# Kernel optimization log

Hardware: AMD Instinct MI355X
Metric: run time of the kernel (lower is better)

The kernel has to match this reference:

```python
import jax, jax.numpy as jnp
import numpy as np

B, T, F, H = 8192, 96, 64, 256


def setup_inputs() -> dict:
    key = jax.random.key(0)
    ks = jax.random.split(key, 8)
    s = 0.05
    return {
        "decoder_feature": jax.random.normal(ks[0], (B, T, F), jnp.float32),
        "init_state": jax.random.normal(ks[1], (B, H), jnp.float32),
        "decoder_init_input": jax.random.normal(ks[2], (B, 1), jnp.float32),
        "kernel": jax.random.normal(ks[3], (1 + F, 3 * H), jnp.float32) * s,
        "recurrent_kernel": jax.random.normal(ks[4], (H, 3 * H), jnp.float32) * s,
        "input_bias": jnp.zeros((3 * H,), jnp.float32),
        "recurrent_bias": jnp.zeros((3 * H,), jnp.float32),
        "dense_w": jax.random.normal(ks[5], (H, 1), jnp.float32) * s,
        "dense_b": jnp.zeros((1,), jnp.float32),
        "predict_seq_length": T,
    }


def reference(decoder_feature, init_state, decoder_init_input, kernel,
              recurrent_kernel, input_bias, recurrent_bias, dense_w, dense_b,
              predict_seq_length):
    # teacher=None, use_attention=False path of Decoder2.forward.
    # Keras GRUCell (reset_after=True) recurrence, scanned over time.
    feats = jnp.swapaxes(decoder_feature[:, :predict_seq_length, :], 0, 1)  # [T,B,F]

    def step(carry, feat_t):
        prev_out, h = carry                                   # [B,1], [B,H]
        x = jnp.concatenate([prev_out, feat_t], axis=-1)      # [B,1+F]
        mx = x @ kernel + input_bias                          # [B,3H]
        mh = h @ recurrent_kernel + recurrent_bias            # [B,3H]
        xz, xr, xh = jnp.split(mx, 3, axis=-1)
        hz, hr, hh = jnp.split(mh, 3, axis=-1)
        z = jax.nn.sigmoid(xz + hz)
        r = jax.nn.sigmoid(xr + hr)
        cand = jnp.tanh(xh + r * hh)
        h_new = z * h + (1.0 - z) * cand
        out = h_new @ dense_w + dense_b                       # [B,1]
        return (out, h_new), out

    _, outs = jax.lax.scan(step, (decoder_init_input, init_state), feats)
    return jnp.swapaxes(outs, 0, 1)                           # [B,T,1]
```

## Files before the change

### kernel.cpp

```cpp
#include <hip/hip_runtime.h>


#define Bdim 8192
#define Tdim 96
#define Fdim 64
#define Hdim 256
#define BM   32
#define XS   72
#define HS   264
#define OS   97

typedef __attribute__((ext_vector_type(8))) short s16x8;
typedef __attribute__((ext_vector_type(4))) float f32x4;

#define MFMA __builtin_amdgcn_mfma_f32_16x16x32_bf16

__device__ __forceinline__ unsigned short f2bf(float f) {
    union { float f; unsigned u; } v; v.f = f;
    unsigned r = v.u + 0x7FFFu + ((v.u >> 16) & 1u);
    return (unsigned short)(r >> 16);
}

__global__ void prep_swz(const float* __restrict__ Wk, const float* __restrict__ Wr,
                         unsigned short* __restrict__ sW) {
    int idx = blockIdx.x * blockDim.x + threadIdx.x;
    if (idx >= 480 * 64) return;
    int lane = idx & 63, f = idx >> 6;
    int n2 = f & 1;
    int g  = (f >> 1) % 3;
    int kt = (f / 6) % 10;
    int w  = f / 60;
    int q = lane >> 4, cc = lane & 15;
    int n = g * 256 + w * 32 + n2 * 16 + cc;
    unsigned short* d = sW + (size_t)idx * 8;
#pragma unroll
    for (int j = 0; j < 8; ++j) {
        float v;
        if (kt < 8) v = Wr[(size_t)(kt * 32 + q * 8 + j) * 768 + n];
        else        v = Wk[(size_t)(1 + (kt - 8) * 32 + q * 8 + j) * 768 + n];
        d[j] = f2bf(v);
    }
}

__launch_bounds__(512, 2)
__global__ void gru_mfma5(
    const float* __restrict__ feat,
    const float* __restrict__ init_state,
    const float* __restrict__ init_inp,
    const unsigned short* __restrict__ sW,
    const float* __restrict__ Wk,
    const float* __restrict__ ib, const float* __restrict__ rb,
    const float* __restrict__ dw, const float* __restrict__ db,
    float* __restrict__ out)
{
    __shared__ __align__(16) unsigned short xs[BM * XS];
    __shared__ __align__(16) unsigned short hs[BM * HS];
    __shared__ float wpart[2][8][BM];
    __shared__ float outbuf[BM * OS];

    const int tid  = threadIdx.x;
    const int lane = tid & 63;
    const int w    = tid >> 6;
    const int q    = lane >> 4;
    const int c    = lane & 15;
    const int b0   = blockIdx.x * BM;

    float bz[2], brr[2], bxh[2], bhh[2], wk0z[2], wk0r[2], wk0h[2], dwv[2];
#pragma unroll
    for (int n2 = 0; n2 < 2; ++n2) {
        int col = w * 32 + n2 * 16 + c;
        bz[n2]   = ib[col]       + rb[col];
        brr[n2]  = ib[256 + col] + rb[256 + col];
        bxh[n2]  = ib[512 + col];
        bhh[n2]  = rb[512 + col];
        wk0z[n2] = Wk[col];
        wk0r[n2] = Wk[256 + col];
        wk0h[n2] = Wk[512 + col];
        dwv[n2]  = dw[col];
    }
    const float dbv = db[0];

    float hreg[2][2][4];
    float prevreg[2][4];
#pragma unroll
    for (int mt = 0; mt < 2; ++mt)
#pragma unroll
        for (int i = 0; i < 4; ++i) {
            int row = mt * 16 + q * 4 + i;
            prevreg[mt][i] = init_inp[b0 + row];
#pragma unroll
            for (int n2 = 0; n2 < 2; ++n2) {
                int col = w * 32 + n2 * 16 + c;
                float v = init_state[(size_t)(b0 + row) * Hdim + col];
                hreg[mt][n2][i] = v;
                hs[row * HS + col] = f2bf(v);
            }
        }

    {
        int r = tid >> 4, fi = tid & 15;
        float4 f = *(const float4*)&feat[((size_t)(b0 + r) * Tdim + 0) * Fdim + fi * 4];
        ushort4 p; p.x = f2bf(f.x); p.y = f2bf(f.y); p.z = f2bf(f.z); p.w = f2bf(f.w);
        *(ushort4*)&xs[r * XS + fi * 4] = p;
    }

    const unsigned short* wp0 = sW + (size_t)(w * 60) * 512 + lane * 8;

    __syncthreads();

    for (int t = 0; t < Tdim; ++t) {
        f32x4 az[2][2], arr[2][2], axh[2][2], ahh[2][2];
#pragma unroll
        for (int mt = 0; mt < 2; ++mt)
#pragma unroll
            for (int n2 = 0; n2 < 2; ++n2) {
                az[mt][n2] = (f32x4)0.0f; arr[mt][n2] = (f32x4)0.0f;
                axh[mt][n2] = (f32x4)0.0f; ahh[mt][n2] = (f32x4)0.0f;
            }

#pragma unroll
        for (int kt = 0; kt < 10; ++kt) {
            const unsigned short* fp = wp0 + (size_t)(kt * 6) * 512;
            s16x8 b00 = *(const s16x8*)(fp + 0 * 512);
            s16x8 b01 = *(const s16x8*)(fp + 1 * 512);
            s16x8 b10 = *(const s16x8*)(fp + 2 * 512);
            s16x8 b11 = *(const s16x8*)(fp + 3 * 512);
            s16x8 b20 = *(const s16x8*)(fp + 4 * 512);
            s16x8 b21 = *(const s16x8*)(fp + 5 * 512);
            s16x8 a0, a1;
            if (kt < 8) {
                a0 = *(const s16x8*)&hs[c * HS + kt * 32 + q * 8];
                a1 = *(const s16x8*)&hs[(16 + c) * HS + kt * 32 + q * 8];
            } else {
                a0 = *(const s16x8*)&xs[c * XS + (kt - 8) * 32 + q * 8];
                a1 = *(const s16x8*)&xs[(16 + c) * XS + (kt - 8) * 32 + q * 8];
            }
            az[0][0]  = MFMA(a0, b00, az[0][0], 0, 0, 0);
            az[1][0]  = MFMA(a1, b00, az[1][0], 0, 0, 0);
            az[0][1]  = MFMA(a0, b01, az[0][1], 0, 0, 0);
            az[1][1]  = MFMA(a1, b01, az[1][1], 0, 0, 0);
            arr[0][0] = MFMA(a0, b10, arr[0][0], 0, 0, 0);
            arr[1][0] = MFMA(a1, b10, arr[1][0], 0, 0, 0);
            arr[0][1] = MFMA(a0, b11, arr[0][1], 0, 0, 0);
            arr[1][1] = MFMA(a1, b11, arr[1][1], 0, 0, 0);
            if (kt < 8) {
                ahh[0][0] = MFMA(a0, b20, ahh[0][0], 0, 0, 0);
                ahh[1][0] = MFMA(a1, b20, ahh[1][0], 0, 0, 0);
                ahh[0][1] = MFMA(a0, b21, ahh[0][1], 0, 0, 0);
                ahh[1][1] = MFMA(a1, b21, ahh[1][1], 0, 0, 0);
            } else {
                axh[0][0] = MFMA(a0, b20, axh[0][0], 0, 0, 0);
                axh[1][0] = MFMA(a1, b20, axh[1][0], 0, 0, 0);
                axh[0][1] = MFMA(a0, b21, axh[0][1], 0, 0, 0);
                axh[1][1] = MFMA(a1, b21, axh[1][1], 0, 0, 0);
            }
        }
        __syncthreads();

        if (t > 0) {
            int r = lane & 31;
            float s = dbv;
            const float (*wp)[BM] = wpart[(t - 1) & 1];
#pragma unroll
            for (int ww = 0; ww < 8; ++ww) s += wp[ww][r];
            if (w == 0 && lane < 32) outbuf[r * OS + (t - 1)] = s;
#pragma unroll
            for (int mt = 0; mt < 2; ++mt)
#pragma unroll
                for (int i = 0; i < 4; ++i)
                    prevreg[mt][i] = __shfl(s, mt * 16 + q * 4 + i, 64);
        }

        float sd[2][4];
#pragma unroll
        for (int mt = 0; mt < 2; ++mt)
#pragma unroll
            for (int i = 0; i < 4; ++i) sd[mt][i] = 0.0f;

#pragma unroll
        for (int mt = 0; mt < 2; ++mt)
#pragma unroll
            for (int n2 = 0; n2 < 2; ++n2)
#pragma unroll
                for (int i = 0; i < 4; ++i) {
                    float pv = prevreg[mt][i];
                    float zz = 1.0f / (1.0f + __expf(-(az[mt][n2][i] + bz[n2] + pv * wk0z[n2])));
                    float rr = 1.0f / (1.0f + __expf(-(arr[mt][n2][i] + brr[n2] + pv * wk0r[n2])));
                    float cd = tanhf(axh[mt][n2][i] + bxh[n2] + pv * wk0h[n2] +
                                     rr * (ahh[mt][n2][i] + bhh[n2]));
                    float hn = zz * hreg[mt][n2][i] + (1.0f - zz) * cd;
                    hreg[mt][n2][i] = hn;
                    hs[(mt * 16 + q * 4 + i) * HS + w * 32 + n2 * 16 + c] = f2bf(hn);
                    sd[mt][i] += hn * dwv[n2];
                }

#pragma unroll
        for (int mt = 0; mt < 2; ++mt)
#pragma unroll
            for (int i = 0; i < 4; ++i) {
                float s = sd[mt][i];
                s += __shfl_xor(s, 1, 64);
                s += __shfl_xor(s, 2, 64);
                s += __shfl_xor(s, 4, 64);
                s += __shfl_xor(s, 8, 64);
                if (c == 0) wpart[t & 1][w][mt * 16 + q * 4 + i] = s;
            }

        if (t + 1 < Tdim) {
            int r = tid >> 4, fi = tid & 15;
            float4 f = *(const float4*)&feat[((size_t)(b0 + r) * Tdim + (t + 1)) * Fdim + fi * 4];
            ushort4 p; p.x = f2bf(f.x); p.y = f2bf(f.y); p.z = f2bf(f.z); p.w = f2bf(f.w);
            *(ushort4*)&xs[r * XS + fi * 4] = p;
        }
        __syncthreads();
    }

    {
        int r = lane & 31;
        float s = dbv;
        const float (*wp)[BM] = wpart[(Tdim - 1) & 1];
#pragma unroll
        for (int ww = 0; ww < 8; ++ww) s += wp[ww][r];
        if (w == 0 && lane < 32) outbuf[r * OS + (Tdim - 1)] = s;
    }
    __syncthreads();

    for (int i = tid; i < BM * Tdim; i += 512) {
        int r = i / Tdim, tt = i - r * Tdim;
        out[(size_t)b0 * Tdim + i] = outbuf[r * OS + tt];
    }
}

extern "C" void kernel_launch(void* const* d_in, const int* in_sizes, int n_in,
                              void* d_out, int out_size, void* d_ws, size_t ws_size,
                              hipStream_t stream) {
    const float* feat       = (const float*)d_in[0];
    const float* init_state = (const float*)d_in[1];
    const float* init_inp   = (const float*)d_in[2];
    const float* Wk         = (const float*)d_in[3];
    const float* Wr         = (const float*)d_in[4];
    const float* ib         = (const float*)d_in[5];
    const float* rb         = (const float*)d_in[6];
    const float* dw         = (const float*)d_in[7];
    const float* db         = (const float*)d_in[8];
    float* out              = (float*)d_out;

    unsigned short* sW = (unsigned short*)d_ws;

    prep_swz<<<120, 256, 0, stream>>>(Wk, Wr, sW);
    gru_mfma5<<<Bdim / BM, 512, 0, stream>>>(
        feat, init_state, init_inp, sW, Wk, ib, rb, dw, db, out);
}
```

Before: 1.727 ms.

## Halve batch tile to 16 rows with 4 waves each owning 64 hidden columns

Changes the GRU block from 32 batch rows and 8 waves to 16 rows and 4 waves, each wave now computing 64 hidden columns across all three gates. The weight swizzle is re-laid out to match, so each wave issues more MFMAs per A-fragment and the grid doubles to 512 blocks. Biases and the previous-output term are now folded into the accumulator initialisation, and the previous-output reduction moves to the start of the step. The cost is that every block re-streams the full weight matrix from global/L2 for half as many rows, doubling weight traffic per batch element, while register pressure rises from 12 B-fragments held per k-step.

```diff
diff --git a/kernel.cpp b/kernel.cpp
--- a/kernel.cpp
+++ b/kernel.cpp
@@ -5,7 +5,7 @@
 #define Tdim 96
 #define Fdim 64
 #define Hdim 256
-#define BM   32
+#define BM   16
 #define XS   72
 #define HS   264
 #define OS   97
@@ -26,12 +26,12 @@
     int idx = blockIdx.x * blockDim.x + threadIdx.x;
     if (idx >= 480 * 64) return;
     int lane = idx & 63, f = idx >> 6;
-    int n2 = f & 1;
-    int g  = (f >> 1) % 3;
-    int kt = (f / 6) % 10;
-    int w  = f / 60;
+    int n4 = f & 3;
+    int g  = (f >> 2) % 3;
+    int kt = (f / 12) % 10;
+    int w  = f / 120;
     int q = lane >> 4, cc = lane & 15;
-    int n = g * 256 + w * 32 + n2 * 16 + cc;
+    int n = g * 256 + w * 64 + n4 * 16 + cc;
     unsigned short* d = sW + (size_t)idx * 8;
 #pragma unroll
     for (int j = 0; j < 8; ++j) {
@@ -42,8 +42,8 @@
     }
 }
 
-__launch_bounds__(512, 2)
-__global__ void gru_mfma5(
+__launch_bounds__(256)
+__global__ void gru_mfma7(
     const float* __restrict__ feat,
     const float* __restrict__ init_state,
     const float* __restrict__ init_inp,
@@ -55,8 +55,12 @@
 {
     __shared__ __align__(16) unsigned short xs[BM * XS];
     __shared__ __align__(16) unsigned short hs[BM * HS];
-    __shared__ float wpart[2][8][BM];
+    __shared__ float wpart[2][4][BM];
     __shared__ float outbuf[BM * OS];
+    __shared__ float wk0s[768];
+    __shared__ float dws[Hdim];
+    __shared__ float biasL[1024];
+    __shared__ float prevs[BM];
 
     const int tid  = threadIdx.x;
     const int lane = tid & 63;
@@ -65,36 +69,28 @@
     const int c    = lane & 15;
     const int b0   = blockIdx.x * BM;
 
-    float bz[2], brr[2], bxh[2], bhh[2], wk0z[2], wk0r[2], wk0h[2], dwv[2];
-#pragma unroll
-    for (int n2 = 0; n2 < 2; ++n2) {
-        int col = w * 32 + n2 * 16 + c;
-        bz[n2]   = ib[col]       + rb[col];
-        brr[n2]  = ib[256 + col] + rb[256 + col];
-        bxh[n2]  = ib[512 + col];
-        bhh[n2]  = rb[512 + col];
-        wk0z[n2] = Wk[col];
-        wk0r[n2] = Wk[256 + col];
-        wk0h[n2] = Wk[512 + col];
-        dwv[n2]  = dw[col];
-    }
+    for (int i = tid; i < 768; i += 256) wk0s[i] = Wk[i];
+    dws[tid] = dw[tid];
+    {
+        int i = tid;
+        biasL[i]       = ib[i]       + rb[i];
+        biasL[256 + i] = ib[256 + i] + rb[256 + i];
+        biasL[512 + i] = ib[512 + i];
+        biasL[768 + i] = rb[512 + i];
+    }
+    if (tid < BM) prevs[tid] = init_inp[b0 + tid];
     const float dbv = db[0];
 
-    float hreg[2][2][4];
-    float prevreg[2][4];
-#pragma unroll
-    for (int mt = 0; mt < 2; ++mt)
+    float hreg[4][4];
+#pragma unroll
+    for (int n4 = 0; n4 < 4; ++n4)
 #pragma unroll
         for (int i = 0; i < 4; ++i) {
-            int row = mt * 16 + q * 4 + i;
-            prevreg[mt][i] = init_inp[b0 + row];
-#pragma unroll
-            for (int n2 = 0; n2 < 2; ++n2) {
-                int col = w * 32 + n2 * 16 + c;
-                float v = init_state[(size_t)(b0 + row) * Hdim + col];
-                hreg[mt][n2][i] = v;
-                hs[row * HS + col] = f2bf(v);
-            }
+            int row = q * 4 + i;
+            int col = w * 64 + n4 * 16 + c;
+            float v = init_state[(size_t)(b0 + row) * Hdim + col];
+            hreg[n4][i] = v;
+            hs[row * HS + col] = f2bf(v);
         }
 
     {
@@ -104,107 +100,88 @@
         *(ushort4*)&xs[r * XS + fi * 4] = p;
     }
 
-    const unsigned short* wp0 = sW + (size_t)(w * 60) * 512 + lane * 8;
+    const unsigned short* wp0 = sW + (size_t)(w * 120) * 512 + lane * 8;
 
     __syncthreads();
 
     for (int t = 0; t < Tdim; ++t) {
-        f32x4 az[2][2], arr[2][2], axh[2][2], ahh[2][2];
-#pragma unroll
-        for (int mt = 0; mt < 2; ++mt)
-#pragma unroll
-            for (int n2 = 0; n2 < 2; ++n2) {
-                az[mt][n2] = (f32x4)0.0f; arr[mt][n2] = (f32x4)0.0f;
-                axh[mt][n2] = (f32x4)0.0f; ahh[mt][n2] = (f32x4)0.0f;
+        float pv[4];
+        if (t == 0) {
+#pragma unroll
+            for (int i = 0; i < 4; ++i) pv[i] = prevs[q * 4 + i];
+        } else {
+            int r = lane & 15;
+            const float (*wp)[BM] = wpart[(t - 1) & 1];
+            float s = dbv + wp[0][r] + wp[1][r] + wp[2][r] + wp[3][r];
+            if (w == 0 && lane < BM) outbuf[r * OS + (t - 1)] = s;
+#pragma unroll
+            for (int i = 0; i < 4; ++i) pv[i] = __shfl(s, q * 4 + i, 64);
+        }
+
+        f32x4 az[4], arr[4], axh[4], ahh[4];
+#pragma unroll
+        for (int n4 = 0; n4 < 4; ++n4) {
+            int col = w * 64 + n4 * 16 + c;
+            float bzv = biasL[col], brv = biasL[256 + col];
+            float bxv = biasL[512 + col], bhv = biasL[768 + col];
+            float wz = wk0s[col], wr_ = wk0s[256 + col], wh = wk0s[512 + col];
+#pragma unroll
+            for (int i = 0; i < 4; ++i) {
+                az[n4][i]  = bzv + pv[i] * wz;
+                arr[n4][i] = brv + pv[i] * wr_;
+                axh[n4][i] = bxv + pv[i] * wh;
+                ahh[n4][i] = bhv;
             }
+        }
 
 #pragma unroll
         for (int kt = 0; kt < 10; ++kt) {
-            const unsigned short* fp = wp0 + (size_t)(kt * 6) * 512;
-            s16x8 b00 = *(const s16x8*)(fp + 0 * 512);
-            s16x8 b01 = *(const s16x8*)(fp + 1 * 512);
-            s16x8 b10 = *(const s16x8*)(fp + 2 * 512);
-            s16x8 b11 = *(const s16x8*)(fp + 3 * 512);
-            s16x8 b20 = *(const s16x8*)(fp + 4 * 512);
-            s16x8 b21 = *(const s16x8*)(fp + 5 * 512);
-            s16x8 a0, a1;
+            const unsigned short* fp = wp0 + (size_t)(kt * 12) * 512;
+            s16x8 b[12];
+#pragma unroll
+            for (int u = 0; u < 12; ++u) b[u] = *(const s16x8*)(fp + u * 512);
+            s16x8 a;
+            if (kt < 8) a = *(const s16x8*)&hs[c * HS + kt * 32 + q * 8];
+            else        a = *(const s16x8*)&xs[c * XS + (kt - 8) * 32 + q * 8];
+#pragma unroll
+            for (int n4 = 0; n4 < 4; ++n4) az[n4]  = MFMA(a, b[n4],     az[n4], 0, 0, 0);
+#pragma unroll
+            for (int n4 = 0; n4 < 4; ++n4) arr[n4] = MFMA(a, b[4 + n4], arr[n4], 0, 0, 0);
             if (kt < 8) {
-                a0 = *(const s16x8*)&hs[c * HS + kt * 32 + q * 8];
-                a1 = *(const s16x8*)&hs[(16 + c) * HS + kt * 32 + q * 8];
+#pragma unroll
+                for (int n4 = 0; n4 < 4; ++n4) ahh[n4] = MFMA(a, b[8 + n4], ahh[n4], 0, 0, 0);
             } else {
-                a0 = *(const s16x8*)&xs[c * XS + (kt - 8) * 32 + q * 8];
-                a1 = *(const s16x8*)&xs[(16 + c) * XS + (kt - 8) * 32 + q * 8];
+#pragma unroll
+                for (int n4 = 0; n4 < 4; ++n4) axh[n4] = MFMA(a, b[8 + n4], axh[n4], 0, 0, 0);
             }
-            az[0][0]  = MFMA(a0, b00, az[0][0], 0, 0, 0);
-            az[1][0]  = MFMA(a1, b00, az[1][0], 0, 0, 0);
-            az[0][1]  = MFMA(a0, b01, az[0][1], 0, 0, 0);
-            az[1][1]  = MFMA(a1, b01, az[1][1], 0, 0, 0);
-            arr[0][0] = MFMA(a0, b10, arr[0][0], 0, 0, 0);
-            arr[1][0] = MFMA(a1, b10, arr[1][0], 0, 0, 0);
-            arr[0][1] = MFMA(a0, b11, arr[0][1], 0, 0, 0);
-            arr[1][1] = MFMA(a1, b11, arr[1][1], 0, 0, 0);
-            if (kt < 8) {
-                ahh[0][0] = MFMA(a0, b20, ahh[0][0], 0, 0, 0);
-                ahh[1][0] = MFMA(a1, b20, ahh[1][0], 0, 0, 0);
-                ahh[0][1] = MFMA(a0, b21, ahh[0][1], 0, 0, 0);
-                ahh[1][1] = MFMA(a1, b21, ahh[1][1], 0, 0, 0);
-            } else {
-                axh[0][0] = MFMA(a0, b20, axh[0][0], 0, 0, 0);
-                axh[1][0] = MFMA(a1, b20, axh[1][0], 0, 0, 0);
-                axh[0][1] = MFMA(a0, b21, axh[0][1], 0, 0, 0);
-                axh[1][1] = MFMA(a1, b21, axh[1][1], 0, 0, 0);
+        }
+        __syncthreads();
+
+        float sd[4] = {0.0f, 0.0f, 0.0f, 0.0f};
+#pragma unroll
+        for (int n4 = 0; n4 < 4; ++n4) {
+            int col = w * 64 + n4 * 16 + c;
+            float dv = dws[col];
+#pragma unroll
+            for (int i = 0; i < 4; ++i) {
+                float zz = 1.0f / (1.0f + __expf(-az[n4][i]));
+                float rr = 1.0f / (1.0f + __expf(-arr[n4][i]));
+                float cd = tanhf(axh[n4][i] + rr * ahh[n4][i]);
+                float hn = zz * hreg[n4][i] + (1.0f - zz) * cd;
+                hreg[n4][i] = hn;
+                hs[(q * 4 + i) * HS + col] = f2bf(hn);
+                sd[i] += hn * dv;
             }
         }
-        __syncthreads();
-
-        if (t > 0) {
-            int r = lane & 31;
-            float s = dbv;
-            const float (*wp)[BM] = wpart[(t - 1) & 1];
-#pragma unroll
-            for (int ww = 0; ww < 8; ++ww) s += wp[ww][r];
-            if (w == 0 && lane < 32) outbuf[r * OS + (t - 1)] = s;
-#pragma unroll
-            for (int mt = 0; mt < 2; ++mt)
-#pragma unroll
-                for (int i = 0; i < 4; ++i)
-                    prevreg[mt][i] = __shfl(s, mt * 16 + q * 4 + i, 64);
-        }
-
-        float sd[2][4];
-#pragma unroll
-        for (int mt = 0; mt < 2; ++mt)
-#pragma unroll
-            for (int i = 0; i < 4; ++i) sd[mt][i] = 0.0f;
-
-#pragma unroll
-        for (int mt = 0; mt < 2; ++mt)
-#pragma unroll
-            for (int n2 = 0; n2 < 2; ++n2)
-#pragma unroll
-                for (int i = 0; i < 4; ++i) {
-                    float pv = prevreg[mt][i];
-                    float zz = 1.0f / (1.0f + __expf(-(az[mt][n2][i] + bz[n2] + pv * wk0z[n2])));
-                    float rr = 1.0f / (1.0f + __expf(-(arr[mt][n2][i] + brr[n2] + pv * wk0r[n2])));
-                    float cd = tanhf(axh[mt][n2][i] + bxh[n2] + pv * wk0h[n2] +
-                                     rr * (ahh[mt][n2][i] + bhh[n2]));
-                    float hn = zz * hreg[mt][n2][i] + (1.0f - zz) * cd;
-                    hreg[mt][n2][i] = hn;
-                    hs[(mt * 16 + q * 4 + i) * HS + w * 32 + n2 * 16 + c] = f2bf(hn);
-                    sd[mt][i] += hn * dwv[n2];
-                }
-
-#pragma unroll
-        for (int mt = 0; mt < 2; ++mt)
-#pragma unroll
-            for (int i = 0; i < 4; ++i) {
-                float s = sd[mt][i];
-                s += __shfl_xor(s, 1, 64);
-                s += __shfl_xor(s, 2, 64);
-                s += __shfl_xor(s, 4, 64);
-                s += __shfl_xor(s, 8, 64);
-                if (c == 0) wpart[t & 1][w][mt * 16 + q * 4 + i] = s;
-            }
+#pragma unroll
+        for (int i = 0; i < 4; ++i) {
+            float s = sd[i];
+            s += __shfl_xor(s, 1, 64);
+            s += __shfl_xor(s, 2, 64);
+            s += __shfl_xor(s, 4, 64);
+            s += __shfl_xor(s, 8, 64);
+            if (c == 0) wpart[t & 1][w][q * 4 + i] = s;
+        }
 
         if (t + 1 < Tdim) {
             int r = tid >> 4, fi = tid & 15;
@@ -216,16 +193,14 @@
     }
 
     {
-        int r = lane & 31;
-        float s = dbv;
+        int r = lane & 15;
         const float (*wp)[BM] = wpart[(Tdim - 1) & 1];
-#pragma unroll
-        for (int ww = 0; ww < 8; ++ww) s += wp[ww][r];
-        if (w == 0 && lane < 32) outbuf[r * OS + (Tdim - 1)] = s;
+        float s = dbv + wp[0][r] + wp[1][r] + wp[2][r] + wp[3][r];
+        if (w == 0 && lane < BM) outbuf[r * OS + (Tdim - 1)] = s;
     }
     __syncthreads();
 
-    for (int i = tid; i < BM * Tdim; i += 512) {
+    for (int i = tid; i < BM * Tdim; i += 256) {
         int r = i / Tdim, tt = i - r * Tdim;
         out[(size_t)b0 * Tdim + i] = outbuf[r * OS + tt];
     }
@@ -248,6 +223,6 @@
     unsigned short* sW = (unsigned short*)d_ws;
 
     prep_swz<<<120, 256, 0, stream>>>(Wk, Wr, sW);
-    gru_mfma5<<<Bdim / BM, 512, 0, stream>>>(
+    gru_mfma7<<<Bdim / BM, 256, 0, stream>>>(
         feat, init_state, init_inp, sW, Wk, ib, rb, dw, db, out);
 }
```

Result: slower. 2.480 ms (+43.6%).
